# Kernel optimization log

Measured on AMD Instinct MI355X. Metric: run time of the kernel, lower is better.

The kernel has to match this reference:

```python
import jax, jax.numpy as jnp
import numpy as np

# LIF hyperparameters (from the torch module's `parameters` dict)
C = 1.0            # C_Osc
THR = 1.0          # v_Osc_threshold
BS = 256           # trials_per_stimulus
N = 512            # neurons_n
N_IN = 512         # n_in
TAU_SYN = 0.01     # tau_Osc_Ie
TAU_SYN_REC = 0.01 # tau_Osc_Irec
TAU_NEU = 0.02     # tau_Osc
GAIN_SYN = 1.0     # TDE_to_Osc_current
GAIN_SYN_REC = 0.5 # gain_syn_rec
DT = 0.001         # clock_sim
VR = 0.0           # reset_osc
I_MIN = 0.0        # I_minimum_osc
I_STEP = 0.01      # I_step_osc
REFRAC = 0.002     # refrac_Osc
REFR = REFRAC / DT # refractory period in steps
T = 500            # simulated timesteps


def spike(x):
    # SurrGradSpike.forward: hard threshold (surrogate grad only matters in bwd)
    return (x > 0.0).astype(x.dtype)


def setup_inputs() -> dict:
    key = jax.random.key(0)
    k1, k2, k3 = jax.random.split(key, 3)
    x = jax.random.uniform(k1, (T, BS, N_IN), dtype=jnp.float32)
    # train=True init: h1 ~ N(1, (std*0.5/sqrt(n_in))^2), r1 ~ N(0, same)
    std = 1.0 * 0.5 / np.sqrt(N_IN)
    h1 = 1.0 + std * jax.random.normal(k2, (N_IN, N), dtype=jnp.float32)
    r1 = std * jax.random.normal(k3, (N, N), dtype=jnp.float32)
    return {"x": x, "h1": h1, "r1": r1}


def reference(x, h1, r1):
    steady = I_MIN + I_STEP * jnp.arange(N, dtype=jnp.float32)  # [N]

    def step(state, x_t):
        V, Isyn, Irec, cnt, spk = state
        Isyn = Isyn - DT * Isyn / TAU_SYN + GAIN_SYN * (x_t @ h1)
        Irec = Irec - DT * Irec / TAU_SYN_REC + GAIN_SYN_REC * (spk @ r1)
        V = V + DT * (-V / TAU_NEU + (Isyn + Irec + steady) / C)
        V = jnp.maximum(V, 0.0)
        spk_new = spike(V - THR)
        cnt = REFR * spk_new + (1.0 - spk_new) * (cnt - 1.0)
        V = (1.0 - spk_new) * V * (cnt <= 0.0).astype(V.dtype) + spk_new * VR
        return (V, Isyn, Irec, cnt, spk_new), spk_new

    init = (
        jnp.ones((BS, N), jnp.float32),   # V
        jnp.zeros((BS, N), jnp.float32),  # Isyn
        jnp.zeros((BS, N), jnp.float32),  # Irec
        jnp.zeros((BS, N), jnp.float32),  # count_refr
        jnp.zeros((BS, N), jnp.float32),  # spk
    )
    _, spikes = jax.lax.scan(step, init, x)
    return spikes  # [T, BS, N]
```

## Files before the change

kernel.cpp:

```cpp
#include <hip/hip_runtime.h>

typedef __attribute__((ext_vector_type(8))) short short8;
typedef __attribute__((ext_vector_type(4))) float f32x4;

constexpr int BSZ = 256;
constexpr int NRN = 512;
constexpr int KIN = 512;
constexpr int TT  = 500;
constexpr int BM  = 128;
constexpr int BN  = 128;
constexpr int KT  = 32;
constexpr int NBLK = (TT * BSZ / BM) * (NRN / BN);
constexpr size_t WS_NEED = (size_t)2 * KIN * NRN * sizeof(unsigned short);

__device__ __forceinline__ unsigned short bf16rne(float f) {
    unsigned u = __float_as_uint(f);
    u += 0x7FFFu + ((u >> 16) & 1u);
    return (unsigned short)(u >> 16);
}
__device__ __forceinline__ float bf16f(unsigned short s) {
    return __uint_as_float(((unsigned)s) << 16);
}
__device__ __forceinline__ unsigned cvtpk(float a, float b) {
    unsigned r;
    asm("v_cvt_pk_bf16_f32 %0, %1, %2" : "=v"(r) : "v"(a), "v"(b));
    return r;
}

__global__ __launch_bounds__(512)
void split_h(const float* __restrict__ h1,
             unsigned short* __restrict__ wsH,
             unsigned short* __restrict__ wsL)
{
    const int k = blockIdx.x;
    const int n = threadIdx.x;
    const float v = h1[(size_t)k * NRN + n];
    const unsigned short h  = bf16rne(v);
    const unsigned short lo = bf16rne(v - bf16f(h));
    const int kt = k >> 5, koct = (k >> 3) & 3, i = k & 7;
    const int nb = n >> 7, nl = n & 127;
    const int byte = (kt * 4 + nb) * 8192 +
                     ((nl * 64 + koct * 16) ^ (((nl >> 1) & 3) << 4)) + i * 2;
    *reinterpret_cast<unsigned short*>((char*)wsH + byte) = h;
    *reinterpret_cast<unsigned short*>((char*)wsL + byte) = lo;
}

template<bool PS>
__global__ __launch_bounds__(256)
void lif_gemm(const float* __restrict__ x,
              const float* __restrict__ h1,
              const unsigned short* __restrict__ wsH,
              const unsigned short* __restrict__ wsL,
              float* __restrict__ out)
{
    __shared__ short AhS[BM * KT], AlS[BM * KT], BhS[BN * KT], BlS[BN * KT];

    const int tid  = threadIdx.x;
    const int l    = tid & 63;
    const int w    = tid >> 6;
    const int wm   = (w & 1) * 64;
    const int wn   = (w >> 1) * 64;
    const int lrow = l & 15;
    const int loct = l >> 4;

    const int nid = (blockIdx.x & 7) * (NBLK / 8) + (blockIdx.x >> 3);
    const size_t m0 = (size_t)(nid >> 2) * BM;
    const int    nb = nid & 3;
    const int    n0 = nb * BN;

    f32x4 acc[4][4];
    #pragma unroll
    for (int i = 0; i < 4; ++i)
        #pragma unroll
        for (int j = 0; j < 4; ++j) acc[i][j] = (f32x4)0.0f;

    for (int kt = 0; kt < KIN / KT; ++kt) {
        if (PS) {
            const float4* sH = reinterpret_cast<const float4*>(
                (const char*)wsH + (kt * 4 + nb) * 8192);
            const float4* sL = reinterpret_cast<const float4*>(
                (const char*)wsL + (kt * 4 + nb) * 8192);
            float4* dH = reinterpret_cast<float4*>(BhS);
            float4* dL = reinterpret_cast<float4*>(BlS);
            dH[tid]       = sH[tid];
            dH[256 + tid] = sH[256 + tid];
            dL[tid]       = sL[tid];
            dL[256 + tid] = sL[256 + tid];
        } else {
            #pragma unroll
            for (int u2 = 0; u2 < 2; ++u2) {
                const int u = u2 * 256 + tid;
                const int nl = u & 127, koct = u >> 7;
                short8 hh, hl;
                #pragma unroll
                for (int i = 0; i < 8; ++i) {
                    const float v = h1[(size_t)(kt * KT + koct * 8 + i) * NRN + n0 + nl];
                    const unsigned short h = bf16rne(v);
                    hh[i] = (short)h;
                    hl[i] = (short)bf16rne(v - bf16f(h));
                }
                const int byte = (nl * 64 + koct * 16) ^ (((nl >> 1) & 3) << 4);
                *reinterpret_cast<short8*>((char*)BhS + byte) = hh;
                *reinterpret_cast<short8*>((char*)BlS + byte) = hl;
            }
        }
        #pragma unroll
        for (int u4 = 0; u4 < 4; ++u4) {
            const int u = u4 * 256 + tid;
            const int row = u >> 3, slot = u & 7;
            const float4 xv = *reinterpret_cast<const float4*>(
                x + (m0 + row) * KIN + kt * KT + slot * 4);
            const unsigned h01 = cvtpk(xv.x, xv.y);
            const unsigned h23 = cvtpk(xv.z, xv.w);
            const float r0 = xv.x - __uint_as_float(h01 << 16);
            const float r1v = xv.y - __uint_as_float(h01 & 0xFFFF0000u);
            const float r2 = xv.z - __uint_as_float(h23 << 16);
            const float r3 = xv.w - __uint_as_float(h23 & 0xFFFF0000u);
            const unsigned l01 = cvtpk(r0, r1v);
            const unsigned l23 = cvtpk(r2, r3);
            const unsigned long long hb = (unsigned long long)h01 | ((unsigned long long)h23 << 32);
            const unsigned long long lb = (unsigned long long)l01 | ((unsigned long long)l23 << 32);
            const int byte = (row * 64 + slot * 8) ^ (((row >> 1) & 3) << 4);
            *reinterpret_cast<unsigned long long*>((char*)AhS + byte) = hb;
            *reinterpret_cast<unsigned long long*>((char*)AlS + byte) = lb;
        }
        __syncthreads();

        short8 ah[4], al[4], bh[4], bl[4];
        #pragma unroll
        for (int mi = 0; mi < 4; ++mi) {
            const int row  = wm + mi * 16 + lrow;
            const int byte = (row * 64 + loct * 16) ^ (((row >> 1) & 3) << 4);
            ah[mi] = *reinterpret_cast<const short8*>((const char*)AhS + byte);
            al[mi] = *reinterpret_cast<const short8*>((const char*)AlS + byte);
        }
        #pragma unroll
        for (int ni = 0; ni < 4; ++ni) {
            const int nn   = wn + ni * 16 + lrow;
            const int byte = (nn * 64 + loct * 16) ^ (((nn >> 1) & 3) << 4);
            bh[ni] = *reinterpret_cast<const short8*>((const char*)BhS + byte);
            bl[ni] = *reinterpret_cast<const short8*>((const char*)BlS + byte);
        }

        __builtin_amdgcn_s_setprio(1);
        #pragma unroll
        for (int mi = 0; mi < 4; ++mi)
            #pragma unroll
            for (int ni = 0; ni < 4; ++ni) {
                acc[mi][ni] = __builtin_amdgcn_mfma_f32_16x16x32_bf16(ah[mi], bh[ni], acc[mi][ni], 0, 0, 0);
                acc[mi][ni] = __builtin_amdgcn_mfma_f32_16x16x32_bf16(ah[mi], bl[ni], acc[mi][ni], 0, 0, 0);
                acc[mi][ni] = __builtin_amdgcn_mfma_f32_16x16x32_bf16(al[mi], bh[ni], acc[mi][ni], 0, 0, 0);
            }
        __builtin_amdgcn_s_setprio(0);
        __syncthreads();
    }

    #pragma unroll
    for (int mi = 0; mi < 4; ++mi)
        #pragma unroll
        for (int j = 0; j < 4; ++j) {
            const size_t row = m0 + wm + mi * 16 + loct * 4 + j;
            float* op = out + row * NRN + n0 + wn + lrow;
            #pragma unroll
            for (int ni = 0; ni < 4; ++ni)
                op[ni * 16] = acc[mi][ni][j];
        }
}

__global__ __launch_bounds__(512, 2)
void lif_scan(const float* __restrict__ r1,
              float* __restrict__ out)
{
    __shared__ unsigned long long smask[2][8];

    const int n  = threadIdx.x;
    const int b  = blockIdx.x;
    const int wv = n >> 6;
    const int ln = n & 63;
    const size_t row = (size_t)b * NRN + n;
    constexpr size_t STEP = (size_t)BSZ * NRN;

    if (n < 16) ((unsigned long long*)smask)[n] = 0ULL;

    double csum = 0.0;
    for (int j = 0; j < KIN; ++j)
        csum += (double)r1[(size_t)j * NRN + n];

    double V = 1.0, Is = 0.0, Ir = 0.0, cnt = 0.0;
    const double steady = 0.01 * (double)n;
    constexpr double kS = 0.1, kN = 0.05, DT = 0.001;

    float a0 = out[0 * STEP + row];
    float a1 = out[1 * STEP + row];
    float a2 = out[2 * STEP + row];
    float a3 = out[3 * STEP + row];
    __syncthreads();

#define LIF_STEP(T, AREG)                                                     \
    {                                                                         \
        const int t_ = (T);                                                   \
        const int p_ = t_ & 1;                                                \
        unsigned long long mw[8];                                             \
        int pc = 0;                                                           \
        _Pragma("unroll")                                                     \
        for (int w = 0; w < 8; ++w) { mw[w] = smask[p_][w]; pc += __popcll(mw[w]); } \
        double aR;                                                            \
        if (pc == 512) {                                                      \
            aR = csum;                                                        \
        } else if (pc == 0) {                                                 \
            aR = 0.0;                                                         \
        } else {                                                              \
            aR = 0.0;                                                         \
            _Pragma("unroll")                                                 \
            for (int w = 0; w < 8; ++w) {                                     \
                unsigned long long m_ = mw[w];                                \
                while (m_) {                                 \
                    const int j = w * 64 + __builtin_ctzll(m_);               \
                    aR += (double)r1[(size_t)j * NRN + n];                    \
                    m_ &= m_ - 1;                                             \
                }                                                             \
            }                                                                 \
        }                                                                     \
        Is = Is - kS * Is + (double)(AREG);                 \
        Ir = Ir - kS * Ir + 0.5 * aR;                       \
        double Vn = V - kN * V + DT * (Is + Ir + steady);                     \
        Vn = fmax(Vn, 0.0);                                                   \
        const bool sp = (Vn - 1.0) > 0.0;                                     \
        cnt = sp ? 2.0 : (cnt - 1.0);                           \
        V = sp ? 0.0 : ((cnt <= 0.0) ? Vn : 0.0);                             \
        out[(size_t)t_ * STEP + row] = sp ? 1.0f : 0.0f;                      \
        const unsigned long long bal = __ballot(sp);                          \
        if (ln == 0) smask[p_ ^ 1][wv] = bal;                                 \
        __syncthreads();                                                      \
    }

    for (int t4 = 0; t4 < TT; t4 += 4) {
        LIF_STEP(t4 + 0, a0)
        a0 = (t4 + 4 < TT) ? out[(size_t)(t4 + 4) * STEP + row] : 0.0f;
        LIF_STEP(t4 + 1, a1)
        a1 = (t4 + 5 < TT) ? out[(size_t)(t4 + 5) * STEP + row] : 0.0f;
        LIF_STEP(t4 + 2, a2)
        a2 = (t4 + 6 < TT) ? out[(size_t)(t4 + 6) * STEP + row] : 0.0f;
        LIF_STEP(t4 + 3, a3)
        a3 = (t4 + 7 < TT) ? out[(size_t)(t4 + 7) * STEP + row] : 0.0f;
    }
#undef LIF_STEP
}

extern "C" void kernel_launch(void* const* d_in, const int* in_sizes, int n_in,
                              void* d_out, int out_size, void* d_ws, size_t ws_size,
                              hipStream_t stream) {
    const float* x  = (const float*)d_in[0];
    const float* h1 = (const float*)d_in[1];
    const float* r1 = (const float*)d_in[2];
    float* out = (float*)d_out;
    (void)in_sizes; (void)n_in; (void)out_size;

    if (ws_size >= WS_NEED) {
        unsigned short* wsH = (unsigned short*)d_ws;
        unsigned short* wsL = wsH + (size_t)KIN * NRN;
        split_h<<<dim3(KIN), dim3(NRN), 0, stream>>>(h1, wsH, wsL);
        lif_gemm<true><<<dim3(NBLK), dim3(256), 0, stream>>>(x, h1, wsH, wsL, out);
    } else {
        lif_gemm<false><<<dim3(NBLK), dim3(256), 0, stream>>>(x, h1, nullptr, nullptr, out);
    }
    lif_scan<<<dim3(BSZ), dim3(512), 0, stream>>>(r1, out);
}
```

Baseline: 399.4 us.

## Run LIF scan with one wavefront per batch row, eight neurons per lane

The recurrent scan kernel moves from 512 threads per batch row, which shared spikes through LDS and needed a __syncthreads per timestep, to a single 64-lane wavefront where each lane owns 8 interleaved neurons. Spike masks are built with eight in-register ballots, so no block barrier or shared memory is needed. Loads and stores of r1 and the drive/output use float4 vectors. In exchange each lane does 8x the serial double-precision work and sparse-spike gathers per step, and only 256 wavefronts run in total, which lowers occupancy and latency hiding.

After: 662.0 us. +65.7%, slower.

```diff
diff --git a/kernel.cpp b/kernel.cpp
--- a/kernel.cpp
+++ b/kernel.cpp
@@ -167,82 +167,122 @@
         }
 }
 
-__global__ __launch_bounds__(512, 2)
+__global__ __launch_bounds__(64)
 void lif_scan(const float* __restrict__ r1,
               float* __restrict__ out)
 {
-    __shared__ unsigned long long smask[2][8];
-
-    const int n  = threadIdx.x;
+    const int ln = threadIdx.x;
     const int b  = blockIdx.x;
-    const int wv = n >> 6;
-    const int ln = n & 63;
-    const size_t row = (size_t)b * NRN + n;
+    const int n0 = ln * 8;
     constexpr size_t STEP = (size_t)BSZ * NRN;
-
-    if (n < 16) ((unsigned long long*)smask)[n] = 0ULL;
-
-    double csum = 0.0;
-    for (int j = 0; j < KIN; ++j)
-        csum += (double)r1[(size_t)j * NRN + n];
-
-    double V = 1.0, Is = 0.0, Ir = 0.0, cnt = 0.0;
-    const double steady = 0.01 * (double)n;
+    const size_t rowb = (size_t)b * NRN + n0;
+
+    double csum[8], V[8], Is[8], Ir[8], cnt[8], steady[8];
+    #pragma unroll
+    for (int q = 0; q < 8; ++q) {
+        csum[q] = 0.0; V[q] = 1.0; Is[q] = 0.0; Ir[q] = 0.0; cnt[q] = 0.0;
+        steady[q] = 0.01 * (double)(n0 + q);
+    }
+    for (int j = 0; j < KIN; ++j) {
+        const float4 ra = *reinterpret_cast<const float4*>(r1 + (size_t)j * NRN + n0);
+        const float4 rb = *reinterpret_cast<const float4*>(r1 + (size_t)j * NRN + n0 + 4);
+        csum[0] += (double)ra.x; csum[1] += (double)ra.y;
+        csum[2] += (double)ra.z; csum[3] += (double)ra.w;
+        csum[4] += (double)rb.x; csum[5] += (double)rb.y;
+        csum[6] += (double)rb.z; csum[7] += (double)rb.w;
+    }
+
+    unsigned long long mw[8];
+    #pragma unroll
+    for (int q = 0; q < 8; ++q) mw[q] = 0ULL;
+
     constexpr double kS = 0.1, kN = 0.05, DT = 0.001;
 
-    float a0 = out[0 * STEP + row];
-    float a1 = out[1 * STEP + row];
-    float a2 = out[2 * STEP + row];
-    float a3 = out[3 * STEP + row];
-    __syncthreads();
-
-#define LIF_STEP(T, AREG)                                                     \
+    float4 p0a, p0b, p1a, p1b, p2a, p2b, p3a, p3b;
+    p0a = *reinterpret_cast<const float4*>(out + 0 * STEP + rowb);
+    p0b = *reinterpret_cast<const float4*>(out + 0 * STEP + rowb + 4);
+    p1a = *reinterpret_cast<const float4*>(out + 1 * STEP + rowb);
+    p1b = *reinterpret_cast<const float4*>(out + 1 * STEP + rowb + 4);
+    p2a = *reinterpret_cast<const float4*>(out + 2 * STEP + rowb);
+    p2b = *reinterpret_cast<const float4*>(out + 2 * STEP + rowb + 4);
+    p3a = *reinterpret_cast<const float4*>(out + 3 * STEP + rowb);
+    p3b = *reinterpret_cast<const float4*>(out + 3 * STEP + rowb + 4);
+
+#define LIF_STEP(T, PA, PB)                                                   \
     {                                                                         \
         const int t_ = (T);                                                   \
-        const int p_ = t_ & 1;                                                \
-        unsigned long long mw[8];                                             \
         int pc = 0;                                                           \
         _Pragma("unroll")                                                     \
-        for (int w = 0; w < 8; ++w) { mw[w] = smask[p_][w]; pc += __popcll(mw[w]); } \
-        double aR;                                                            \
+        for (int q = 0; q < 8; ++q) pc += __popcll(mw[q]);                    \
+        double aR[8];                                                         \
         if (pc == 512) {                                                      \
-            aR = csum;                                                        \
+            _Pragma("unroll") for (int q = 0; q < 8; ++q) aR[q] = csum[q];    \
         } else if (pc == 0) {                                                 \
-            aR = 0.0;                                                         \
+            _Pragma("unroll") for (int q = 0; q < 8; ++q) aR[q] = 0.0;        \
         } else {                                                              \
-            aR = 0.0;                                                         \
+            _Pragma("unroll") for (int q = 0; q < 8; ++q) aR[q] = 0.0;        \
             _Pragma("unroll")                                                 \
-            for (int w = 0; w < 8; ++w) {                                     \
-                unsigned long long m_ = mw[w];                                \
-                while (m_) {                                 \
-                    const int j = w * 64 + __builtin_ctzll(m_);               \
-                    aR += (double)r1[(size_t)j * NRN + n];                    \
+            for (int q2 = 0; q2 < 8; ++q2) {                                  \
+                unsigned long long m_ = mw[q2];                               \
+                while (m_) {                           \
+                    const int j = (__builtin_ctzll(m_) << 3) + q2;            \
+                    const float4 ra = *reinterpret_cast<const float4*>(       \
+                        r1 + (size_t)j * NRN + n0);                           \
+                    const float4 rb = *reinterpret_cast<const float4*>(       \
+                        r1 + (size_t)j * NRN + n0 + 4);                       \
+                    aR[0] += (double)ra.x; aR[1] += (double)ra.y;             \
+                    aR[2] += (double)ra.z; aR[3] += (double)ra.w;             \
+                    aR[4] += (double)rb.x; aR[5] += (double)rb.y;             \
+                    aR[6] += (double)rb.z; aR[7] += (double)rb.w;             \
                     m_ &= m_ - 1;                                             \
                 }                                                             \
             }                                                                 \
         }                                                                     \
-        Is = Is - kS * Is + (double)(AREG);                 \
-        Ir = Ir - kS * Ir + 0.5 * aR;                       \
-        double Vn = V - kN * V + DT * (Is + Ir + steady);                     \
-        Vn = fmax(Vn, 0.0);                                                   \
-        const bool sp = (Vn - 1.0) > 0.0;                                     \
-        cnt = sp ? 2.0 : (cnt - 1.0);                           \
-        V = sp ? 0.0 : ((cnt <= 0.0) ? Vn : 0.0);                             \
-        out[(size_t)t_ * STEP + row] = sp ? 1.0f : 0.0f;                      \
-        const unsigned long long bal = __ballot(sp);                          \
-        if (ln == 0) smask[p_ ^ 1][wv] = bal;                                 \
-        __syncthreads();                                                      \
+        const float aSv[8] = { (PA).x, (PA).y, (PA).z, (PA).w,                \
+                               (PB).x, (PB).y, (PB).z, (PB).w };              \
+        float sout[8];                                                        \
+        unsigned spbits = 0;                                                  \
+        _Pragma("unroll")                                                     \
+        for (int q = 0; q < 8; ++q) {                                         \
+            Is[q] = Is[q] - kS * Is[q] + (double)aSv[q];      \
+            Ir[q] = Ir[q] - kS * Ir[q] + 0.5 * aR[q];          \
+            double Vn = V[q] - kN * V[q] + DT * (Is[q] + Ir[q] + steady[q]);  \
+            Vn = fmax(Vn, 0.0);                                               \
+            const bool sp = (Vn - 1.0) > 0.0;                                 \
+            cnt[q] = sp ? 2.0 : (cnt[q] - 1.0);                 \
+            V[q] = sp ? 0.0 : ((cnt[q] <= 0.0) ? Vn : 0.0);                   \
+            sout[q] = sp ? 1.0f : 0.0f;                                       \
+            spbits |= (unsigned)sp << q;                                      \
+        }                                                                     \
+        _Pragma("unroll")                                                     \
+        for (int q = 0; q < 8; ++q) mw[q] = __ballot((spbits >> q) & 1u);     \
+        const float4 o0 = { sout[0], sout[1], sout[2], sout[3] };             \
+        const float4 o1 = { sout[4], sout[5], sout[6], sout[7] };             \
+        *reinterpret_cast<float4*>(out + (size_t)t_ * STEP + rowb)     = o0;  \
+        *reinterpret_cast<float4*>(out + (size_t)t_ * STEP + rowb + 4) = o1;  \
     }
 
     for (int t4 = 0; t4 < TT; t4 += 4) {
-        LIF_STEP(t4 + 0, a0)
-        a0 = (t4 + 4 < TT) ? out[(size_t)(t4 + 4) * STEP + row] : 0.0f;
-        LIF_STEP(t4 + 1, a1)
-        a1 = (t4 + 5 < TT) ? out[(size_t)(t4 + 5) * STEP + row] : 0.0f;
-        LIF_STEP(t4 + 2, a2)
-        a2 = (t4 + 6 < TT) ? out[(size_t)(t4 + 6) * STEP + row] : 0.0f;
-        LIF_STEP(t4 + 3, a3)
-        a3 = (t4 + 7 < TT) ? out[(size_t)(t4 + 7) * STEP + row] : 0.0f;
+        LIF_STEP(t4 + 0, p0a, p0b)
+        if (t4 + 4 < TT) {
+            p0a = *reinterpret_cast<const float4*>(out + (size_t)(t4 + 4) * STEP + rowb);
+            p0b = *reinterpret_cast<const float4*>(out + (size_t)(t4 + 4) * STEP + rowb + 4);
+        }
+        LIF_STEP(t4 + 1, p1a, p1b)
+        if (t4 + 5 < TT) {
+            p1a = *reinterpret_cast<const float4*>(out + (size_t)(t4 + 5) * STEP + rowb);
+            p1b = *reinterpret_cast<const float4*>(out + (size_t)(t4 + 5) * STEP + rowb + 4);
+        }
+        LIF_STEP(t4 + 2, p2a, p2b)
+        if (t4 + 6 < TT) {
+            p2a = *reinterpret_cast<const float4*>(out + (size_t)(t4 + 6) * STEP + rowb);
+            p2b = *reinterpret_cast<const float4*>(out + (size_t)(t4 + 6) * STEP + rowb + 4);
+        }
+        LIF_STEP(t4 + 3, p3a, p3b)
+        if (t4 + 7 < TT) {
+            p3a = *reinterpret_cast<const float4*>(out + (size_t)(t4 + 7) * STEP + rowb);
+            p3b = *reinterpret_cast<const float4*>(out + (size_t)(t4 + 7) * STEP + rowb + 4);
+        }
     }
 #undef LIF_STEP
 }
@@ -264,5 +304,5 @@
     } else {
         lif_gemm<false><<<dim3(NBLK), dim3(256), 0, stream>>>(x, h1, nullptr, nullptr, out);
     }
-    lif_scan<<<dim3(BSZ), dim3(512), 0, stream>>>(r1, out);
-}
+    lif_scan<<<dim3(BSZ), dim3(64), 0, stream>>>(r1, out);
+}
```
